# Kernel optimization log

Measured on AMD Instinct MI355X. Metric: run time of the kernel, lower is better.

## Reference

```python
import jax, jax.numpy as jnp
import numpy as np

N = 8192          # total genes
B = 16            # number of ragged batch groups (equal-size here: 512 each)
D = 768           # hidden_dim
NEG = -1.0e9      # mask fill value used by the original module


def setup_inputs() -> dict:
    key = jax.random.key(0)
    ks = jax.random.split(key, 10)
    s = 0.02
    inp = {
        "gene_embeddings": jax.random.normal(ks[0], (N, D), dtype=jnp.float32),
        # sorted group ids: 16 contiguous groups of 512 genes
        "batch": (jnp.arange(N) // (N // B)).astype(jnp.int64),
        "Wq": jax.random.normal(ks[1], (D, D), dtype=jnp.float32) * s,
        "bq": jnp.zeros((D,), dtype=jnp.float32),
        "Wk": jax.random.normal(ks[2], (D, D), dtype=jnp.float32) * s,
        "bk": jnp.zeros((D,), dtype=jnp.float32),
        "Wv": jax.random.normal(ks[3], (D, D), dtype=jnp.float32) * s,
        "bv": jnp.zeros((D,), dtype=jnp.float32),
        "Wo": jax.random.normal(ks[4], (D, D), dtype=jnp.float32) * s,
        "bo": jnp.zeros((D,), dtype=jnp.float32),
        "beta": jnp.ones((1,), dtype=jnp.float32) * 0.1,
    }
    return inp


def reference(gene_embeddings, batch, Wq, bq, Wk, bk, Wv, bv, Wo, bo, beta):
    # Single-head attention over full hidden_dim (num_heads unused in original).
    x = gene_embeddings
    q = x @ Wq.T + bq                      # [N, D]
    k = x @ Wk.T + bk
    v = x @ Wv.T + bv
    scale = 1.0 / jnp.sqrt(jnp.asarray(D, dtype=x.dtype))
    scores = (q @ k.T) * scale             # [N, N]
    # block-diagonal group mask + diagonal self-mask (same -1e9 fill as torch code)
    same_group = batch[:, None] == batch[None, :]
    eye = jnp.eye(N, dtype=bool)
    allow = same_group & (~eye)
    scores = jnp.where(allow, scores, NEG)
    weights = jax.nn.softmax(scores, axis=-1)   # dropout in eval mode -> identity
    dyn = weights @ v                       # [N, D]
    dyn = dyn @ Wo.T + bo
    return x + beta * dyn
```

## Files before the change

### kernel.cpp

```cpp
#include <hip/hip_runtime.h>
#include <hip/hip_bf16.h>
#include <cstdint>

using u16 = unsigned short;
using u32 = unsigned int;

typedef __bf16 bf16x8 __attribute__((ext_vector_type(8)));
typedef float  f32x4  __attribute__((ext_vector_type(4)));

__device__ __forceinline__ u16 f2b(float f) {
    u32 u = __builtin_bit_cast(u32, f);
    u += 0x7fffu + ((u >> 16) & 1u);
    return (u16)(u >> 16);
}

__device__ __forceinline__ void gload_lds16(const u16* g, u16* l) {
    __builtin_amdgcn_global_load_lds(
        (const __attribute__((address_space(1))) void*)g,
        (__attribute__((address_space(3))) void*)l,
        16, 0, 0);
}

__launch_bounds__(256)
__global__ void pack_kernel(const float* __restrict__ x,
                            const float* __restrict__ Wq,
                            const float* __restrict__ Wk,
                            const float* __restrict__ Wv,
                            const float* __restrict__ Wo,
                            const float* __restrict__ bq,
                            const float* __restrict__ bk,
                            const float* __restrict__ bv,
                            u16* __restrict__ xb,
                            u16* __restrict__ Wqkvb,
                            u16* __restrict__ Wob,
                            float* __restrict__ bqkv)
{
    int c = blockIdx.x * 256 + threadIdx.x;
    long e = (long)c * 8;
    const float* src; u16* dst; long off;
    if (e < 6291456L)      { src = x;  dst = xb;              off = e; }
    else if (e < 6881280L) { src = Wq; dst = Wqkvb;           off = e - 6291456L; }
    else if (e < 7471104L) { src = Wk; dst = Wqkvb + 589824;  off = e - 6881280L; }
    else if (e < 8060928L) { src = Wv; dst = Wqkvb + 1179648; off = e - 7471104L; }
    else                   { src = Wo; dst = Wob;             off = e - 8060928L; }
    float4 v0 = *(const float4*)(src + off);
    float4 v1 = *(const float4*)(src + off + 4);
    union { u16 u[8]; uint4 q; } o;
    o.u[0] = f2b(v0.x); o.u[1] = f2b(v0.y); o.u[2] = f2b(v0.z); o.u[3] = f2b(v0.w);
    o.u[4] = f2b(v1.x); o.u[5] = f2b(v1.y); o.u[6] = f2b(v1.z); o.u[7] = f2b(v1.w);
    *(uint4*)(dst + off) = o.q;
    if (c < 768)        bqkv[c] = bq[c];
    else if (c < 1536)  bqkv[c] = bk[c - 768];
    else if (c < 2304)  bqkv[c] = bv[c - 1536];
}

template<int MODE>
__launch_bounds__(256)
__global__ void gemm_bt(const u16* __restrict__ A, int lda, long sAz,
                        const u16* __restrict__ B, int ldb, long sBz,
                        void* __restrict__ Cv, int ldc, long sCz,
                        int K,
                        const float* __restrict__ bias,
                        const float* __restrict__ xres,
                        const float* __restrict__ betaPtr,
                        float scale,
                        u16* __restrict__ vTout)
{
    __shared__ u16 As[2][128 * 32];
    __shared__ u16 Bs[2][128 * 32];

    const int tid  = threadIdx.x;
    const int g    = blockIdx.z;
    const u16* Ab = A + (long)g * sAz + (long)blockIdx.y * 128 * lda;
    const u16* Bb = B + (long)g * sBz + (long)blockIdx.x * 128 * ldb;

    const int wave = tid >> 6, lane = tid & 63;
    const int wm = (wave >> 1) * 64, wn = (wave & 1) * 64;
    const int ln15 = lane & 15, lq = lane >> 4;

    f32x4 acc[4][4];
#pragma unroll
    for (int i = 0; i < 4; i++)
#pragma unroll
        for (int j = 0; j < 4; j++)
            acc[i][j] = (f32x4){0.f, 0.f, 0.f, 0.f};

    const int c0 = wave * 2, c1 = wave * 2 + 1;
    const int sr0 = c0 * 16 + (lane >> 2), sc = (lane & 3) * 8;
    const int sr1 = c1 * 16 + (lane >> 2);
    const u16* Ag0 = Ab + (long)sr0 * lda + sc;
    const u16* Ag1 = Ab + (long)sr1 * lda + sc;
    const u16* Bg0 = Bb + (long)sr0 * ldb + sc;
    const u16* Bg1 = Bb + (long)sr1 * ldb + sc;

    const int nk = K >> 5;

    gload_lds16(Ag0, &As[0][c0 * 512]);
    gload_lds16(Ag1, &As[0][c1 * 512]);
    gload_lds16(Bg0, &Bs[0][c0 * 512]);
    gload_lds16(Bg1, &Bs[0][c1 * 512]);

    for (int kt = 0; kt < nk; kt++) {
        const int cur = kt & 1;
        __syncthreads();
        if (kt + 1 < nk) {
            const int k0 = (kt + 1) * 32, nxt = cur ^ 1;
            gload_lds16(Ag0 + k0, &As[nxt][c0 * 512]);
            gload_lds16(Ag1 + k0, &As[nxt][c1 * 512]);
            gload_lds16(Bg0 + k0, &Bs[nxt][c0 * 512]);
            gload_lds16(Bg1 + k0, &Bs[nxt][c1 * 512]);
        }

        bf16x8 af[4], bfr[4];
#pragma unroll
        for (int i = 0; i < 4; i++)
            af[i] = *(const bf16x8*)&As[cur][(wm + i * 16 + ln15) * 32 + lq * 8];
#pragma unroll
        for (int j = 0; j < 4; j++)
            bfr[j] = *(const bf16x8*)&Bs[cur][(wn + j * 16 + ln15) * 32 + lq * 8];
#pragma unroll
        for (int i = 0; i < 4; i++)
#pragma unroll
            for (int j = 0; j < 4; j++)
                acc[i][j] = __builtin_amdgcn_mfma_f32_16x16x32_bf16(af[i], bfr[j], acc[i][j], 0, 0, 0);
    }

    const int baseRow = blockIdx.y * 128 + wm;
    const int baseCol = blockIdx.x * 128 + wn;

    if constexpr (MODE == 0) {
        if (baseCol < 1536) {
            u16* C = (u16*)Cv;
#pragma unroll
            for (int i = 0; i < 4; i++)
#pragma unroll
                for (int j = 0; j < 4; j++)
#pragma unroll
                    for (int r = 0; r < 4; r++) {
                        int row = baseRow + i * 16 + lq * 4 + r;
                        int col = baseCol + j * 16 + ln15;
                        C[(long)row * ldc + col] = f2b(acc[i][j][r] + bias[col]);
                    }
        } else {
#pragma unroll
            for (int i = 0; i < 4; i++)
#pragma unroll
                for (int j = 0; j < 4; j++) {
                    int col = baseCol + j * 16 + ln15;
                    float bb = bias[col];
                    ushort4 o;
                    o.x = f2b(acc[i][j][0] + bb);
                    o.y = f2b(acc[i][j][1] + bb);
                    o.z = f2b(acc[i][j][2] + bb);
                    o.w = f2b(acc[i][j][3] + bb);
                    *(ushort4*)(vTout + (long)(col - 1536) * 8192
                                + baseRow + i * 16 + lq * 4) = o;
                }
        }
    } else if constexpr (MODE == 2) {
        float* C = (float*)Cv + (long)g * sCz;
#pragma unroll
        for (int i = 0; i < 4; i++)
#pragma unroll
            for (int j = 0; j < 4; j++)
#pragma unroll
                for (int r = 0; r < 4; r++) {
                    int row = baseRow + i * 16 + lq * 4 + r;
                    int col = baseCol + j * 16 + ln15;
                    float v = acc[i][j][r] * scale;
                    if (row == col) v = -1.0e9f;
                    C[(long)row * ldc + col] = v;
                }
    } else if constexpr (MODE == 3) {
        u16* C = (u16*)Cv + (long)g * sCz;
#pragma unroll
        for (int i = 0; i < 4; i++)
#pragma unroll
            for (int j = 0; j < 4; j++)
#pragma unroll
                for (int r = 0; r < 4; r++) {
                    int row = baseRow + i * 16 + lq * 4 + r;
                    int col = baseCol + j * 16 + ln15;
                    C[(long)row * ldc + col] = f2b(acc[i][j][r]);
                }
    } else {
        float* C = (float*)Cv;
        float bet = betaPtr[0];
#pragma unroll
        for (int i = 0; i < 4; i++)
#pragma unroll
            for (int j = 0; j < 4; j++)
#pragma unroll
                for (int r = 0; r < 4; r++) {
                    int row = baseRow + i * 16 + lq * 4 + r;
                    int col = baseCol + j * 16 + ln15;
                    float v = xres[(long)row * ldc + col] + bet * (acc[i][j][r] + bias[col]);
                    C[(long)row * ldc + col] = v;
                }
    }
}

__launch_bounds__(256)
__global__ void softmax_rows(const float* __restrict__ S, u16* __restrict__ P)
{
    int row  = blockIdx.x * 4 + (threadIdx.x >> 6);
    int lane = threadIdx.x & 63;
    const float* s = S + (long)row * 512 + lane * 8;
    float4 v0 = *(const float4*)s;
    float4 v1 = *(const float4*)(s + 4);
    float vv[8] = {v0.x, v0.y, v0.z, v0.w, v1.x, v1.y, v1.z, v1.w};
    float m = vv[0];
#pragma unroll
    for (int i = 1; i < 8; i++) m = fmaxf(m, vv[i]);
#pragma unroll
    for (int off = 32; off; off >>= 1) m = fmaxf(m, __shfl_xor(m, off));
    float e[8], sum = 0.f;
#pragma unroll
    for (int i = 0; i < 8; i++) { e[i] = __expf(vv[i] - m); sum += e[i]; }
#pragma unroll
    for (int off = 32; off; off >>= 1) sum += __shfl_xor(sum, off);
    float inv = 1.0f / sum;
    union { u16 u[8]; uint4 q; } o;
#pragma unroll
    for (int i = 0; i < 8; i++) o.u[i] = f2b(e[i] * inv);
    *(uint4*)(P + (long)row * 512 + lane * 8) = o.q;
}

extern "C" void kernel_launch(void* const* d_in, const int* in_sizes, int n_in,
                              void* d_out, int out_size, void* d_ws, size_t ws_size,
                              hipStream_t stream)
{
    const float* x    = (const float*)d_in[0];
    const float* Wq   = (const float*)d_in[2];
    const float* bq   = (const float*)d_in[3];
    const float* Wk   = (const float*)d_in[4];
    const float* bk   = (const float*)d_in[5];
    const float* Wv   = (const float*)d_in[6];
    const float* bv   = (const float*)d_in[7];
    const float* Wo   = (const float*)d_in[8];
    const float* bo   = (const float*)d_in[9];
    const float* beta = (const float*)d_in[10];
    float* out = (float*)d_out;

    char* ws = (char*)d_ws;
    u16*   qk    = (u16*)(ws + 0);
    u16*   dyn   = (u16*)(ws + 0);
    u16*   vT    = (u16*)(ws + 25165824);
    u16*   Wqkvb = (u16*)(ws + 37748736);
    u16*   Wob   = (u16*)(ws + 41287680);
    float* bqkv  = (float*)(ws + 42467328);
    u16*   xb    = (u16*)(ws + 42476544);
    float* S     = (float*)(ws + 42476544);
    u16*   P     = (u16*)(ws + 59253760);

    const float scale = 0.03608439182435161f;

    pack_kernel<<<4224, 256, 0, stream>>>(x, Wq, Wk, Wv, Wo, bq, bk, bv,
                                          xb, Wqkvb, Wob, bqkv);

    gemm_bt<0><<<dim3(18, 64, 1), 256, 0, stream>>>(
        xb, 768, 0, Wqkvb, 768, 0, (void*)qk, 1536, 0, 768, bqkv, nullptr, nullptr, 0.f, vT);

    gemm_bt<2><<<dim3(4, 4, 16), 256, 0, stream>>>(
        qk, 1536, 512L * 1536, qk + 768, 1536, 512L * 1536,
        (void*)S, 512, 512L * 512, 768, nullptr, nullptr, nullptr, scale, nullptr);

    softmax_rows<<<2048, 256, 0, stream>>>(S, P);

    gemm_bt<3><<<dim3(6, 4, 16), 256, 0, stream>>>(
        P, 512, 512L * 512, vT, 8192, 512L,
        (void*)dyn, 768, 512L * 768, 512, nullptr, nullptr, nullptr, 0.f, nullptr);

    gemm_bt<4><<<dim3(6, 64, 1), 256, 0, stream>>>(
        dyn, 768, 0, Wob, 768, 0, (void*)out, 768, 0, 768, bo, x, beta, 0.f, nullptr);
}
```

Before: 220.6 us.

## Fuse QK^T, softmax and PV into one per-group attention kernel

Replaces the three-launch attention path (scores GEMM writing fp32 S, row softmax writing bf16 P, PV GEMM) with a single kernel. Each block handles 32 query rows of one group, keeps scores in registers, does a block-level max and sum reduction through LDS, writes unnormalized bf16 probabilities into swizzled LDS, then streams V tiles with double buffering and scales by the inverse sum at the end. This removes the global round trips of the 512x512 score and probability matrices and two launches. In exchange it uses only 256 blocks at one block per CU with 64KB of LDS, so parallelism and latency hiding may be limited.

```diff
diff --git a/kernel.cpp b/kernel.cpp
--- a/kernel.cpp
+++ b/kernel.cpp
@@ -157,32 +157,6 @@
                                 + baseRow + i * 16 + lq * 4) = o;
                 }
         }
-    } else if constexpr (MODE == 2) {
-        float* C = (float*)Cv + (long)g * sCz;
-#pragma unroll
-        for (int i = 0; i < 4; i++)
-#pragma unroll
-            for (int j = 0; j < 4; j++)
-#pragma unroll
-                for (int r = 0; r < 4; r++) {
-                    int row = baseRow + i * 16 + lq * 4 + r;
-                    int col = baseCol + j * 16 + ln15;
-                    float v = acc[i][j][r] * scale;
-                    if (row == col) v = -1.0e9f;
-                    C[(long)row * ldc + col] = v;
-                }
-    } else if constexpr (MODE == 3) {
-        u16* C = (u16*)Cv + (long)g * sCz;
-#pragma unroll
-        for (int i = 0; i < 4; i++)
-#pragma unroll
-            for (int j = 0; j < 4; j++)
-#pragma unroll
-                for (int r = 0; r < 4; r++) {
-                    int row = baseRow + i * 16 + lq * 4 + r;
-                    int col = baseCol + j * 16 + ln15;
-                    C[(long)row * ldc + col] = f2b(acc[i][j][r]);
-                }
     } else {
         float* C = (float*)Cv;
         float bet = betaPtr[0];
@@ -200,30 +174,222 @@
     }
 }
 
-__launch_bounds__(256)
-__global__ void softmax_rows(const float* __restrict__ S, u16* __restrict__ P)
+__launch_bounds__(256, 1)
+__global__ void attn_fused(const u16* __restrict__ qk,
+                           const u16* __restrict__ vT,
+                           u16* __restrict__ dyn,
+                           float scale)
 {
-    int row  = blockIdx.x * 4 + (threadIdx.x >> 6);
-    int lane = threadIdx.x & 63;
-    const float* s = S + (long)row * 512 + lane * 8;
-    float4 v0 = *(const float4*)s;
-    float4 v1 = *(const float4*)(s + 4);
-    float vv[8] = {v0.x, v0.y, v0.z, v0.w, v1.x, v1.y, v1.z, v1.w};
-    float m = vv[0];
-#pragma unroll
-    for (int i = 1; i < 8; i++) m = fmaxf(m, vv[i]);
-#pragma unroll
-    for (int off = 32; off; off >>= 1) m = fmaxf(m, __shfl_xor(m, off));
-    float e[8], sum = 0.f;
-#pragma unroll
-    for (int i = 0; i < 8; i++) { e[i] = __expf(vv[i] - m); sum += e[i]; }
-#pragma unroll
-    for (int off = 32; off; off >>= 1) sum += __shfl_xor(sum, off);
-    float inv = 1.0f / sum;
-    union { u16 u[8]; uint4 q; } o;
-#pragma unroll
-    for (int i = 0; i < 8; i++) o.u[i] = f2b(e[i] * inv);
-    *(uint4*)(P + (long)row * 512 + lane * 8) = o.q;
+    __shared__ char lds[65536];
+    u16* Kb0 = (u16*)lds;
+    u16* Kb1 = (u16*)(lds + 32768);
+    u16* Pl  = (u16*)lds;
+    float* smax = (float*)(lds + 32768);
+    float* ssum = (float*)(lds + 33280);
+    u16* Vb0 = (u16*)(lds + 33792);
+    u16* Vb1 = (u16*)(lds + 46080);
+
+    const int g   = blockIdx.x >> 4;
+    const int mt  = blockIdx.x & 15;
+    const int tid = threadIdx.x;
+    const int wave = tid >> 6, lane = tid & 63;
+    const int ln15 = lane & 15, lq = lane >> 4;
+
+    const int srow = lane >> 2;
+    const int scol = ((lane & 3) ^ ((lane >> 3) & 3)) * 8;
+
+    const long grow0 = (long)g * 512;
+
+    f32x4 accS[2][8];
+#pragma unroll
+    for (int i = 0; i < 2; i++)
+#pragma unroll
+        for (int j = 0; j < 8; j++)
+            accS[i][j] = (f32x4){0.f, 0.f, 0.f, 0.f};
+
+    const u16* Kg[8];
+#pragma unroll
+    for (int t = 0; t < 8; t++)
+        Kg[t] = qk + (grow0 + wave * 128 + t * 16 + srow) * 1536 + 768 + scol;
+
+    const u16* Qg0 = qk + (grow0 + mt * 32 + ln15) * 1536 + lq * 8;
+    const u16* Qg1 = qk + (grow0 + mt * 32 + 16 + ln15) * 1536 + lq * 8;
+
+#pragma unroll
+    for (int t = 0; t < 8; t++)
+        gload_lds16(Kg[t], Kb0 + (wave * 8 + t) * 512);
+
+    for (int kt = 0; kt < 24; kt++) {
+        u16* cur = (kt & 1) ? Kb1 : Kb0;
+        u16* nxt = (kt & 1) ? Kb0 : Kb1;
+        bf16x8 aq0 = *(const bf16x8*)(Qg0 + kt * 32);
+        bf16x8 aq1 = *(const bf16x8*)(Qg1 + kt * 32);
+        __syncthreads();
+        if (kt + 1 < 24) {
+            const int k0 = (kt + 1) * 32;
+#pragma unroll
+            for (int t = 0; t < 8; t++)
+                gload_lds16(Kg[t] + k0, nxt + (wave * 8 + t) * 512);
+        }
+        bf16x8 bk_[8];
+#pragma unroll
+        for (int j = 0; j < 8; j++) {
+            int n = wave * 128 + j * 16 + ln15;
+            int u = n * 4 + (lq ^ ((n >> 1) & 3));
+            bk_[j] = *(const bf16x8*)(cur + u * 8);
+        }
+#pragma unroll
+        for (int j = 0; j < 8; j++) {
+            accS[0][j] = __builtin_amdgcn_mfma_f32_16x16x32_bf16(aq0, bk_[j], accS[0][j], 0, 0, 0);
+            accS[1][j] = __builtin_amdgcn_mfma_f32_16x16x32_bf16(aq1, bk_[j], accS[1][j], 0, 0, 0);
+        }
+    }
+
+    __syncthreads();
+
+    float mr[8];
+#pragma unroll
+    for (int i = 0; i < 2; i++)
+#pragma unroll
+        for (int r = 0; r < 4; r++) {
+            float m = -3.0e38f;
+#pragma unroll
+            for (int j = 0; j < 8; j++) {
+                accS[i][j][r] *= scale;
+                m = fmaxf(m, accS[i][j][r]);
+            }
+            mr[i * 4 + r] = m;
+        }
+#pragma unroll
+    for (int d = 1; d < 16; d <<= 1)
+#pragma unroll
+        for (int k = 0; k < 8; k++)
+            mr[k] = fmaxf(mr[k], __shfl_xor(mr[k], d));
+    if (ln15 == 0) {
+#pragma unroll
+        for (int i = 0; i < 2; i++)
+#pragma unroll
+            for (int r = 0; r < 4; r++)
+                smax[(i * 16 + lq * 4 + r) * 4 + wave] = mr[i * 4 + r];
+    }
+    __syncthreads();
+    float m2[8];
+#pragma unroll
+    for (int i = 0; i < 2; i++)
+#pragma unroll
+        for (int r = 0; r < 4; r++) {
+            float4 v = *(const float4*)&smax[(i * 16 + lq * 4 + r) * 4];
+            m2[i * 4 + r] = fmaxf(fmaxf(v.x, v.y), fmaxf(v.z, v.w));
+        }
+    float sm[8];
+#pragma unroll
+    for (int k = 0; k < 8; k++) sm[k] = 0.f;
+#pragma unroll
+    for (int i = 0; i < 2; i++)
+#pragma unroll
+        for (int j = 0; j < 8; j++)
+#pragma unroll
+            for (int r = 0; r < 4; r++) {
+                int row = i * 16 + lq * 4 + r;
+                int col = wave * 128 + j * 16 + ln15;
+                float e = (mt * 32 + row == col) ? 0.f
+                          : __expf(accS[i][j][r] - m2[i * 4 + r]);
+                sm[i * 4 + r] += e;
+                Pl[row * 512 + (((col >> 3) ^ (row & 7)) << 3) + (col & 7)] = f2b(e);
+            }
+#pragma unroll
+    for (int d = 1; d < 16; d <<= 1)
+#pragma unroll
+        for (int k = 0; k < 8; k++)
+            sm[k] += __shfl_xor(sm[k], d);
+    if (ln15 == 0) {
+#pragma unroll
+        for (int i = 0; i < 2; i++)
+#pragma unroll
+            for (int r = 0; r < 4; r++)
+                ssum[(i * 16 + lq * 4 + r) * 4 + wave] = sm[i * 4 + r];
+    }
+    __syncthreads();
+    float inv[8];
+#pragma unroll
+    for (int i = 0; i < 2; i++)
+#pragma unroll
+        for (int r = 0; r < 4; r++) {
+            float4 v = *(const float4*)&ssum[(i * 16 + lq * 4 + r) * 4];
+            inv[i * 4 + r] = 1.0f / (v.x + v.y + v.z + v.w);
+        }
+
+    f32x4 accO[2][12];
+#pragma unroll
+    for (int i = 0; i < 2; i++)
+#pragma unroll
+        for (int j = 0; j < 12; j++)
+            accO[i][j] = (f32x4){0.f, 0.f, 0.f, 0.f};
+
+    const u16* Vgb = vT + grow0 + scol;
+#define STAGE_V(KT, Q, BUF)                                                   \
+    {                                                                         \
+        _Pragma("unroll")                                                     \
+        for (int t = 0; t < 3; t++) {                                         \
+            int n = (Q) * 192 + (wave * 3 + t) * 16 + srow;                   \
+            gload_lds16(Vgb + (long)n * 8192 + (KT) * 32,                     \
+                        (BUF) + (wave * 3 + t) * 512);                        \
+        }                                                                     \
+    }
+
+    STAGE_V(0, 0, Vb0);
+    bf16x8 ap0, ap1;
+    for (int kt = 0; kt < 16; kt++) {
+#pragma unroll
+        for (int q = 0; q < 4; q++) {
+            u16* curV = (q & 1) ? Vb1 : Vb0;
+            u16* nxtV = (q & 1) ? Vb0 : Vb1;
+            __syncthreads();
+            if (kt * 4 + q + 1 < 64) {
+                int ktn = kt + (q == 3);
+                int qn  = (q + 1) & 3;
+                STAGE_V(ktn, qn, nxtV);
+            }
+            if (q == 0) {
+                {
+                    int row = ln15;
+                    int cu = (kt * 4 + lq) ^ (row & 7);
+                    ap0 = *(const bf16x8*)(Pl + row * 512 + cu * 8);
+                }
+                {
+                    int row = 16 + ln15;
+                    int cu = (kt * 4 + lq) ^ (row & 7);
+                    ap1 = *(const bf16x8*)(Pl + row * 512 + cu * 8);
+                }
+            }
+            bf16x8 bv[3];
+#pragma unroll
+            for (int jj = 0; jj < 3; jj++) {
+                int n = wave * 48 + jj * 16 + ln15;
+                int u = n * 4 + (lq ^ ((n >> 1) & 3));
+                bv[jj] = *(const bf16x8*)(curV + u * 8);
+            }
+#pragma unroll
+            for (int jj = 0; jj < 3; jj++) {
+                accO[0][q * 3 + jj] = __builtin_amdgcn_mfma_f32_16x16x32_bf16(ap0, bv[jj], accO[0][q * 3 + jj], 0, 0, 0);
+                accO[1][q * 3 + jj] = __builtin_amdgcn_mfma_f32_16x16x32_bf16(ap1, bv[jj], accO[1][q * 3 + jj], 0, 0, 0);
+            }
+        }
+    }
+
+#pragma unroll
+    for (int i = 0; i < 2; i++)
+#pragma unroll
+        for (int q = 0; q < 4; q++)
+#pragma unroll
+            for (int jj = 0; jj < 3; jj++)
+#pragma unroll
+                for (int r = 0; r < 4; r++) {
+                    long row = grow0 + mt * 32 + i * 16 + lq * 4 + r;
+                    int col = q * 192 + wave * 48 + jj * 16 + ln15;
+                    dyn[row * 768 + col] = f2b(accO[i][q * 3 + jj][r] * inv[i * 4 + r]);
+                }
+#undef STAGE_V
 }
 
 extern "C" void kernel_launch(void* const* d_in, const int* in_sizes, int n_in,
@@ -244,14 +410,12 @@
 
     char* ws = (char*)d_ws;
     u16*   qk    = (u16*)(ws + 0);
-    u16*   dyn   = (u16*)(ws + 0);
     u16*   vT    = (u16*)(ws + 25165824);
-    u16*   Wqkvb = (u16*)(ws + 37748736);
-    u16*   Wob   = (u16*)(ws + 41287680);
-    float* bqkv  = (float*)(ws + 42467328);
-    u16*   xb    = (u16*)(ws + 42476544);
-    float* S     = (float*)(ws + 42476544);
-    u16*   P     = (u16*)(ws + 59253760);
+    u16*   xb    = (u16*)(ws + 37748736);
+    u16*   dyn   = (u16*)(ws + 37748736);
+    u16*   Wqkvb = (u16*)(ws + 50331648);
+    u16*   Wob   = (u16*)(ws + 53870592);
+    float* bqkv  = (float*)(ws + 55050240);
 
     const float scale = 0.03608439182435161f;
 
@@ -261,15 +425,7 @@
     gemm_bt<0><<<dim3(18, 64, 1), 256, 0, stream>>>(
         xb, 768, 0, Wqkvb, 768, 0, (void*)qk, 1536, 0, 768, bqkv, nullptr, nullptr, 0.f, vT);
 
-    gemm_bt<2><<<dim3(4, 4, 16), 256, 0, stream>>>(
-        qk, 1536, 512L * 1536, qk + 768, 1536, 512L * 1536,
-        (void*)S, 512, 512L * 512, 768, nullptr, nullptr, nullptr, scale, nullptr);
-
-    softmax_rows<<<2048, 256, 0, stream>>>(S, P);
-
-    gemm_bt<3><<<dim3(6, 4, 16), 256, 0, stream>>>(
-        P, 512, 512L * 512, vT, 8192, 512L,
-        (void*)dyn, 768, 512L * 768, 512, nullptr, nullptr, nullptr, 0.f, nullptr);
+    attn_fused<<<256, 256, 0, stream>>>(qk, vT, dyn, scale);
 
     gemm_bt<4><<<dim3(6, 64, 1), 256, 0, stream>>>(
         dyn, 768, 0, Wob, 768, 0, (void*)out, 768, 0, 768, bo, x, beta, 0.f, nullptr);
```

Measured after the change: 230.9 us. 1.05x slower.
